# Kernel tuning notes

Measured on AMD Instinct MI355X. Metric: run time of the kernel, lower is better.

The kernel has to match this reference:

```python
import jax, jax.numpy as jnp
import numpy as np

B, T, S, U = 256, 64, 16, 4  # batch, channels, yt_img_size, upscale_factor


def setup_inputs() -> dict:
    key = jax.random.key(0)
    k1, k2, k3 = jax.random.split(key, 3)
    x = jax.random.normal(k1, (B, T, S, S), dtype=jnp.float32)
    # Stacked per-pixel Linear weights: (P pixels, out=U*U*T, in=T)
    W = jax.random.normal(k2, (S * S, U * U * T, T), dtype=jnp.float32) * 0.05
    b = jax.random.normal(k3, (S * S, U * U * T), dtype=jnp.float32) * 0.01
    return {"x": x, "W": W, "b": b}


def reference(x, W, b):
    Bn, Tn, Sn, _ = x.shape
    P = Sn * Sn
    Un = int(np.sqrt(W.shape[1] // Tn))  # upscale factor, static
    # Per-pixel grouped GEMM: each spatial location has its own Linear(T -> U*U*T)
    xp = x.reshape(Bn, Tn, P).transpose(2, 0, 1)          # (P, B, T)
    y = jnp.einsum('pbt,pot->pbo', xp, W) + b[:, None, :]  # (P, B, U*U*T)
    # Flat output per pixel is viewed as (T, U, U) and scattered to the (i*U:(i+1)*U, j*U:(j+1)*U) patch
    y = y.reshape(Sn, Sn, Bn, Tn, Un, Un)                  # (Si, Sj, B, T, Ui, Uj)
    y = y.transpose(2, 3, 0, 4, 1, 5)                      # (B, T, Si, Ui, Sj, Uj)
    return y.reshape(Bn, Tn, Sn * Un, Sn * Un)
```

## Files before the change

### kernel.cpp

```cpp
#include <hip/hip_runtime.h>
#include <hip/hip_bf16.h>


#define P_PIX 256
#define BATCH 256
#define KDIM 64
#define ODIM 1024

using bf16x8 = __attribute__((ext_vector_type(8))) short;
using f32x4  = __attribute__((ext_vector_type(4))) float;

__global__ __launch_bounds__(256) void transpose_convert(
    const float* __restrict__ x, __hip_bfloat16* __restrict__ xp)
{
    __shared__ float tile[64][65];
    const int R = BATCH * KDIM;
    int p0 = (blockIdx.x & 3) * 64;
    int r0 = (blockIdx.x >> 2) * 64;
    int tp = threadIdx.x & 63;
    int t4 = threadIdx.x >> 6;
    #pragma unroll
    for (int i = 0; i < 16; ++i) {
        int r = t4 + i * 4;
        tile[r][tp] = x[(size_t)(r0 + r) * P_PIX + p0 + tp];
    }
    __syncthreads();
    #pragma unroll
    for (int i = 0; i < 16; ++i) {
        int pl = t4 + i * 4;
        xp[(size_t)(p0 + pl) * R + r0 + tp] = __float2bfloat16(tile[tp][pl]);
    }
}

__device__ __forceinline__ bf16x8 cvt8(f32x4 a, f32x4 b) {
    __hip_bfloat16 h[8];
    h[0] = __float2bfloat16(a[0]); h[1] = __float2bfloat16(a[1]);
    h[2] = __float2bfloat16(a[2]); h[3] = __float2bfloat16(a[3]);
    h[4] = __float2bfloat16(b[0]); h[5] = __float2bfloat16(b[1]);
    h[6] = __float2bfloat16(b[2]); h[7] = __float2bfloat16(b[3]);
    return *(bf16x8*)h;
}

__global__ __launch_bounds__(256, 4) void gemm_pixel_t(
    const __hip_bfloat16* __restrict__ xp,
    const float* __restrict__ W,
    const float* __restrict__ bias,
    float* __restrict__ out)
{
    const int id    = blockIdx.x;
    const int xcd   = id & 7;
    const int l     = id >> 3;
    const int btile = l & 3;
    const int u     = l >> 2;
    const int si    = u >> 3;
    const int t     = (u & 7) * 8 + xcd;
    const int tid   = threadIdx.x;
    const int wave  = tid >> 6;
    const int lane  = tid & 63;
    const int lrow  = lane & 15;
    const int quad  = lane >> 4;
    const int b     = btile * 64 + wave * 16 + lrow;

    const __hip_bfloat16* xr0 = xp + (size_t)(si * 16) * (BATCH * KDIM)
                                   + (size_t)b * KDIM + quad * 8;
    const float* wr0 = W + (size_t)(si * 16) * (ODIM * KDIM)
                         + (size_t)(t * 16 + lrow) * KDIM + quad * 8;
    const float* br0 = bias + (size_t)(si * 16) * ODIM + t * 16 + quad * 4;
    float* orow = out + ((size_t)b * 64 + t) * 4096 + (si * 4 + quad) * 64;

    #pragma unroll
    for (int g = 0; g < 2; ++g) {
        f32x4 acc[8];
        #pragma unroll
        for (int s = 0; s < 8; ++s) {
            const int sj = g * 8 + s;
            const __hip_bfloat16* xr = xr0 + (size_t)sj * (BATCH * KDIM);
            const float*          wr = wr0 + (size_t)sj * (ODIM * KDIM);
            bf16x8 xv0 = *(const bf16x8*)(xr);
            bf16x8 xv1 = *(const bf16x8*)(xr + 32);
            f32x4 w0 = *(const f32x4*)(wr);
            f32x4 w1 = *(const f32x4*)(wr + 4);
            f32x4 w2 = *(const f32x4*)(wr + 32);
            f32x4 w3 = *(const f32x4*)(wr + 36);
            f32x4 c = {};
            c = __builtin_amdgcn_mfma_f32_16x16x32_bf16(cvt8(w0, w1), xv0, c, 0, 0, 0);
            c = __builtin_amdgcn_mfma_f32_16x16x32_bf16(cvt8(w2, w3), xv1, c, 0, 0, 0);
            c += *(const f32x4*)(br0 + (size_t)sj * ODIM);
            acc[s] = c;
        }
        #pragma unroll
        for (int s = 0; s < 8; ++s) {
            *(f32x4*)(orow + (g * 8 + s) * 4) = acc[s];
        }
    }
}

extern "C" void kernel_launch(void* const* d_in, const int* in_sizes, int n_in,
                              void* d_out, int out_size, void* d_ws, size_t ws_size,
                              hipStream_t stream) {
    const float* x    = (const float*)d_in[0];
    const float* W    = (const float*)d_in[1];
    const float* bias = (const float*)d_in[2];
    float* out = (float*)d_out;
    __hip_bfloat16* xp = (__hip_bfloat16*)d_ws;

    transpose_convert<<<1024, 256, 0, stream>>>(x, xp);
    gemm_pixel_t<<<4096, 256, 0, stream>>>(xp, W, bias, out);
}
```

Measured before the change: 572.4 us.

## Stage weights via async global-to-LDS double buffer and coalesce output stores through LDS

The per-pixel GEMM now loads each 16x64 weight tile once per block into swizzled shared memory with global_load_lds, double-buffered across the 16 pixel columns. Before, each of the four waves fetched the same tile separately. Accumulators are staged through a padded per-wave LDS buffer so each lane writes a contiguous 16-byte chunk of the output row instead of scattered ones. The price is a __syncthreads per iteration, extra shared memory that may limit occupancy, and a serialized loop where the old code issued many independent loads at once.

```diff
diff --git a/kernel.cpp b/kernel.cpp
--- a/kernel.cpp
+++ b/kernel.cpp
@@ -9,6 +9,9 @@
 
 using bf16x8 = __attribute__((ext_vector_type(8))) short;
 using f32x4  = __attribute__((ext_vector_type(4))) float;
+
+typedef __attribute__((address_space(1))) const void cv_as1;
+typedef __attribute__((address_space(3))) void v_as3;
 
 __global__ __launch_bounds__(256) void transpose_convert(
     const float* __restrict__ x, __hip_bfloat16* __restrict__ xp)
@@ -41,12 +44,15 @@
     return *(bf16x8*)h;
 }
 
-__global__ __launch_bounds__(256, 4) void gemm_pixel_t(
+__global__ __launch_bounds__(256, 4) void gemm_pixel_v3(
     const __hip_bfloat16* __restrict__ xp,
     const float* __restrict__ W,
     const float* __restrict__ bias,
     float* __restrict__ out)
 {
+    __shared__ float wbuf[2][16 * 64];
+    __shared__ float cbuf[4][16 * 17 * 4];
+
     const int id    = blockIdx.x;
     const int xcd   = id & 7;
     const int l     = id >> 3;
@@ -61,36 +67,65 @@
     const int quad  = lane >> 4;
     const int b     = btile * 64 + wave * 16 + lrow;
 
-    const __hip_bfloat16* xr0 = xp + (size_t)(si * 16) * (BATCH * KDIM)
-                                   + (size_t)b * KDIM + quad * 8;
-    const float* wr0 = W + (size_t)(si * 16) * (ODIM * KDIM)
-                         + (size_t)(t * 16 + lrow) * KDIM + quad * 8;
-    const float* br0 = bias + (size_t)(si * 16) * ODIM + t * 16 + quad * 4;
-    float* orow = out + ((size_t)b * 64 + t) * 4096 + (si * 4 + quad) * 64;
+    const int sr = tid >> 4, sc = tid & 15;
+    const size_t wsrc_chunk = (size_t)(sr * 16 + (sc ^ sr)) * 4;
+
+    f32x4  acc4[4];
+    bf16x8 xA[2], xB[2];
+    f32x4  bv[2];
+
+    {
+        const float* ws = W + ((size_t)(si * 16 + 0) * ODIM + t * 16) * KDIM;
+        __builtin_amdgcn_global_load_lds((cv_as1*)(ws + wsrc_chunk),
+                                         (v_as3*)(&wbuf[0][tid * 4]), 16, 0, 0);
+        const __hip_bfloat16* xs = xp + ((size_t)(si * 16 + 0) * BATCH + b) * KDIM + quad * 8;
+        xA[0] = *(const bf16x8*)(xs);
+        xB[0] = *(const bf16x8*)(xs + 32);
+        bv[0] = *(const f32x4*)(bias + (size_t)(si * 16 + 0) * ODIM + t * 16 + quad * 4);
+    }
 
     #pragma unroll
-    for (int g = 0; g < 2; ++g) {
-        f32x4 acc[8];
-        #pragma unroll
-        for (int s = 0; s < 8; ++s) {
-            const int sj = g * 8 + s;
-            const __hip_bfloat16* xr = xr0 + (size_t)sj * (BATCH * KDIM);
-            const float*          wr = wr0 + (size_t)sj * (ODIM * KDIM);
-            bf16x8 xv0 = *(const bf16x8*)(xr);
-            bf16x8 xv1 = *(const bf16x8*)(xr + 32);
-            f32x4 w0 = *(const f32x4*)(wr);
-            f32x4 w1 = *(const f32x4*)(wr + 4);
-            f32x4 w2 = *(const f32x4*)(wr + 32);
-            f32x4 w3 = *(const f32x4*)(wr + 36);
-            f32x4 c = {};
-            c = __builtin_amdgcn_mfma_f32_16x16x32_bf16(cvt8(w0, w1), xv0, c, 0, 0, 0);
-            c = __builtin_amdgcn_mfma_f32_16x16x32_bf16(cvt8(w2, w3), xv1, c, 0, 0, 0);
-            c += *(const f32x4*)(br0 + (size_t)sj * ODIM);
-            acc[s] = c;
+    for (int sj = 0; sj < 16; ++sj) {
+        const int pb = sj & 1;
+        __syncthreads();
+        if (sj < 15) {
+            const float* ws = W + ((size_t)(si * 16 + sj + 1) * ODIM + t * 16) * KDIM;
+            __builtin_amdgcn_global_load_lds((cv_as1*)(ws + wsrc_chunk),
+                                             (v_as3*)(&wbuf[pb ^ 1][tid * 4]), 16, 0, 0);
+            const __hip_bfloat16* xs = xp + ((size_t)(si * 16 + sj + 1) * BATCH + b) * KDIM + quad * 8;
+            xA[pb ^ 1] = *(const bf16x8*)(xs);
+            xB[pb ^ 1] = *(const bf16x8*)(xs + 32);
+            bv[pb ^ 1] = *(const f32x4*)(bias + (size_t)(si * 16 + sj + 1) * ODIM + t * 16 + quad * 4);
         }
-        #pragma unroll
-        for (int s = 0; s < 8; ++s) {
-            *(f32x4*)(orow + (g * 8 + s) * 4) = acc[s];
+        {
+            const float* wb = wbuf[pb];
+            f32x4 w00 = *(const f32x4*)(wb + (size_t)(lrow * 16 + ((quad * 2 + 0) ^ lrow)) * 4);
+            f32x4 w01 = *(const f32x4*)(wb + (size_t)(lrow * 16 + ((quad * 2 + 1) ^ lrow)) * 4);
+            f32x4 w10 = *(const f32x4*)(wb + (size_t)(lrow * 16 + ((quad * 2 + 8) ^ lrow)) * 4);
+            f32x4 w11 = *(const f32x4*)(wb + (size_t)(lrow * 16 + ((quad * 2 + 9) ^ lrow)) * 4);
+            f32x4 cc = {};
+            cc = __builtin_amdgcn_mfma_f32_16x16x32_bf16(cvt8(w00, w01), xA[pb], cc, 0, 0, 0);
+            cc = __builtin_amdgcn_mfma_f32_16x16x32_bf16(cvt8(w10, w11), xB[pb], cc, 0, 0, 0);
+            acc4[sj & 3] = cc + bv[pb];
+        }
+        if ((sj & 3) == 3) {
+            const int g = sj >> 2;
+            float* cb = &cbuf[wave][0];
+            *(f32x4*)(cb + (size_t)(lrow * 17 + quad * 4 + 0) * 4) = acc4[0];
+            *(f32x4*)(cb + (size_t)(lrow * 17 + quad * 4 + 1) * 4) = acc4[1];
+            *(f32x4*)(cb + (size_t)(lrow * 17 + quad * 4 + 2) * 4) = acc4[2];
+            *(f32x4*)(cb + (size_t)(lrow * 17 + quad * 4 + 3) * 4) = acc4[3];
+            const int i4  = lane >> 2;
+            const int cch = lane & 3;
+            #pragma unroll
+            for (int j = 0; j < 4; ++j) {
+                const int b_off = j * 4 + (i4 & 3);
+                const int row   = i4 >> 2;
+                f32x4 v = *(const f32x4*)(cb + (size_t)(b_off * 17 + row * 4 + cch) * 4);
+                float* dst = out + ((size_t)(btile * 64 + wave * 16 + b_off) * 64 + t) * 4096
+                                 + (si * 4 + row) * 64 + g * 16 + cch * 4;
+                *(f32x4*)dst = v;
+            }
         }
     }
 }
@@ -105,5 +140,5 @@
     __hip_bfloat16* xp = (__hip_bfloat16*)d_ws;
 
     transpose_convert<<<1024, 256, 0, stream>>>(x, xp);
-    gemm_pixel_t<<<4096, 256, 0, stream>>>(xp, W, bias, out);
+    gemm_pixel_v3<<<4096, 256, 0, stream>>>(xp, W, bias, out);
 }
```

Result: faster. 468.5 us (-18.2%).
